# Kernel tuning notes

Hardware: AMD Instinct MI355X
Metric: run time of the kernel (lower is better)

Reference implementation:

```python
import jax, jax.numpy as jnp
import numpy as np

NEG_SLOPE = 0.2


def _add_self_loops(src, dst, edge_attr, n):
    # PyG add_self_loops with fill_value='mean': self-loop attr for node i is the
    # mean of edge_attr over edges whose target is i (0 if none).
    attr_sum = jax.ops.segment_sum(edge_attr, dst, num_segments=n)          # [N,1]
    cnt = jax.ops.segment_sum(jnp.ones((src.shape[0],), edge_attr.dtype), dst, num_segments=n)
    loop_attr = attr_sum / jnp.maximum(cnt, 1.0)[:, None]                   # [N,1]
    loop = jnp.arange(n, dtype=src.dtype)
    return (jnp.concatenate([src, loop]),
            jnp.concatenate([dst, loop]),
            jnp.concatenate([edge_attr, loop_attr], axis=0))


def _gatv2_layer(x, src, dst, eattr, Wl, Wr, We, att, b, n):
    # GATv2Conv (heads=1, concat=False): e_ij = att . leaky_relu(Wl x_j + Wr x_i + We a_ij)
    xl = x @ Wl                                   # [N,C] source transform
    xr = x @ Wr                                   # [N,C] target transform
    ef = eattr @ We                               # [E,C]
    z = jax.nn.leaky_relu(xl[src] + xr[dst] + ef, NEG_SLOPE)   # [E,C]
    logits = z @ att                              # [E]
    # segment softmax over target node dst
    m = jax.ops.segment_max(logits, dst, num_segments=n)
    ex = jnp.exp(logits - m[dst])
    s = jax.ops.segment_sum(ex, dst, num_segments=n)
    alpha = ex / (s[dst] + 1e-16)                 # [E]
    out = jax.ops.segment_sum(alpha[:, None] * xl[src], dst, num_segments=n)  # [N,C]
    return out + b


def setup_inputs() -> dict:
    key = jax.random.key(0)
    ks = jax.random.split(key, 16)
    N, E, F_IN, H, OUT = 50000, 800000, 128, 128, 64
    x = jax.random.normal(ks[0], (N, F_IN), jnp.float32)
    edge_index = jax.random.randint(ks[1], (2, E), 0, N, jnp.int32)
    edge_attr = jax.random.normal(ks[2], (E, 1), jnp.float32)
    s = 0.1
    return {
        "x": x, "edge_index": edge_index, "edge_attr": edge_attr,
        "Wl1": jax.random.normal(ks[3], (F_IN, H), jnp.float32) * s,
        "Wr1": jax.random.normal(ks[4], (F_IN, H), jnp.float32) * s,
        "We1": jax.random.normal(ks[5], (1, H), jnp.float32) * s,
        "att1": jax.random.normal(ks[6], (H,), jnp.float32) * s,
        "b1": jnp.zeros((H,), jnp.float32),
        "Wl2": jax.random.normal(ks[7], (H, OUT), jnp.float32) * s,
        "Wr2": jax.random.normal(ks[8], (H, OUT), jnp.float32) * s,
        "We2": jax.random.normal(ks[9], (1, OUT), jnp.float32) * s,
        "att2": jax.random.normal(ks[10], (OUT,), jnp.float32) * s,
        "b2": jnp.zeros((OUT,), jnp.float32),
    }


def reference(x, edge_index, edge_attr, Wl1, Wr1, We1, att1, b1, Wl2, Wr2, We2, att2, b2):
    n = x.shape[0]
    src, dst, ea = _add_self_loops(edge_index[0], edge_index[1], edge_attr, n)
    h = jax.nn.elu(_gatv2_layer(x, src, dst, ea, Wl1, Wr1, We1, att1, b1, n))
    out = jax.nn.elu(_gatv2_layer(h, src, dst, ea, Wl2, Wr2, We2, att2, b2, n))
    return out
```

## Files before the change

kernel.cpp:

```cpp
#include <hip/hip_runtime.h>
#include <math.h>


#define NEG_SLOPE 0.2f
#define CNT_SHIFT 44
#define SUM_MASK ((1ULL << 44) - 1)
#define ATTR_BIAS 8.0
#define ATTR_SCALE 268435456.0

typedef __attribute__((ext_vector_type(8))) short bf16x8;
typedef __attribute__((ext_vector_type(4))) float f32x4;

__device__ __forceinline__ float bf_lo(unsigned int u) { return __uint_as_float(u << 16); }
__device__ __forceinline__ float bf_hi(unsigned int u) { return __uint_as_float(u & 0xFFFF0000u); }
__device__ __forceinline__ unsigned short bf16_rne(float f) {
    unsigned int u = __float_as_uint(f);
    return (unsigned short)((u + 0x7FFFu + ((u >> 16) & 1u)) >> 16);
}
__device__ __forceinline__ unsigned int pack_bf16(float a, float b) {
    unsigned int ua = __float_as_uint(a);
    unsigned int ub = __float_as_uint(b);
    ua = (ua + 0x7FFFu + ((ua >> 16) & 1u)) >> 16;
    ub = (ub + 0x7FFFu + ((ub >> 16) & 1u)) & 0xFFFF0000u;
    return ua | ub;
}

__global__ void wprep_kernel(const float* __restrict__ Wl1, const float* __restrict__ Wr1,
                             const float* __restrict__ Wl2, const float* __restrict__ Wr2,
                             short* __restrict__ Wt1, short* __restrict__ Wt2) {
    int i = blockIdx.x * 256 + threadIdx.x;
    if (i < 256 * 128) {
        int nn = i >> 7, k = i & 127;
        float v = (nn < 128) ? Wl1[k * 128 + nn] : Wr1[k * 128 + (nn - 128)];
        Wt1[i] = (short)bf16_rne(v);
    } else if (i < 256 * 128 + 128 * 128) {
        int j = i - 256 * 128;
        int nn = j >> 7, k = j & 127;
        float v = (nn < 64) ? Wl2[k * 64 + nn] : Wr2[k * 64 + (nn - 64)];
        Wt2[j] = (short)bf16_rne(v);
    }
}

__global__ void edge_pass1_kernel(const int* __restrict__ dst, const float* __restrict__ eattr,
                                  unsigned long long* __restrict__ packed,
                                  unsigned short* __restrict__ rank, int E) {
    int e = blockIdx.x * blockDim.x + threadIdx.x;
    if (e < E) {
        int d = dst[e];
        double q = ((double)eattr[e] + ATTR_BIAS) * ATTR_SCALE;
        unsigned long long inc = (1ULL << CNT_SHIFT) | (unsigned long long)q;
        unsigned long long old = atomicAdd(&packed[d], inc);
        rank[e] = (unsigned short)(old >> CNT_SHIFT);
    }
}

__global__ __launch_bounds__(1024) void scan_part_kernel(
    const unsigned long long* __restrict__ packed, int* __restrict__ partials, int n) {
    __shared__ int red[1024];
    int gid = blockIdx.x * 1024 + threadIdx.x;
    red[threadIdx.x] = (gid < n) ? ((int)(packed[gid] >> CNT_SHIFT) + 1) : 0;
    __syncthreads();
    for (int off = 512; off > 0; off >>= 1) {
        if (threadIdx.x < off) red[threadIdx.x] += red[threadIdx.x + off];
        __syncthreads();
    }
    if (threadIdx.x == 0) partials[blockIdx.x] = red[0];
}

__global__ __launch_bounds__(1024) void scan_blocksums_kernel(int* __restrict__ partials, int nb) {
    __shared__ int buf[1024];
    int t = threadIdx.x;
    int v = (t < nb) ? partials[t] : 0;
    buf[t] = v;
    __syncthreads();
    for (int off = 1; off < 1024; off <<= 1) {
        int a = (t >= off) ? buf[t - off] : 0;
        __syncthreads();
        buf[t] += a;
        __syncthreads();
    }
    if (t < nb) partials[t] = buf[t] - v;
}

__global__ __launch_bounds__(1024) void scan_final_kernel(
    const unsigned long long* __restrict__ packed, const int* __restrict__ partials,
    int* __restrict__ row_ptr, int n) {
    __shared__ int buf[1024];
    int gid = blockIdx.x * 1024 + threadIdx.x;
    int v = (gid < n) ? ((int)(packed[gid] >> CNT_SHIFT) + 1) : 0;
    buf[threadIdx.x] = v;
    __syncthreads();
    for (int off = 1; off < 1024; off <<= 1) {
        int a = (threadIdx.x >= off) ? buf[threadIdx.x - off] : 0;
        __syncthreads();
        buf[threadIdx.x] += a;
        __syncthreads();
    }
    if (gid < n) row_ptr[gid + 1] = partials[blockIdx.x] + buf[threadIdx.x];
    if (gid == 0) row_ptr[0] = 0;
}

__global__ void csr_scatter_kernel(const int* __restrict__ src, const int* __restrict__ dst,
                                   const float* __restrict__ eattr,
                                   const unsigned long long* __restrict__ packed,
                                   const unsigned short* __restrict__ rank,
                                   const int* __restrict__ row_ptr,
                                   int2* __restrict__ csr, int E, int n) {
    int i = blockIdx.x * blockDim.x + threadIdx.x;
    if (i < E) {
        int d = dst[i];
        csr[row_ptr[d] + rank[i]] = make_int2(src[i], __float_as_int(eattr[i]));
    } else if (i < E + n) {
        int v = i - E;
        unsigned long long p = packed[v];
        int cnt = (int)(p >> CNT_SHIFT);
        double sum = (double)(p & SUM_MASK) * (1.0 / ATTR_SCALE) - ATTR_BIAS * cnt;
        float mean = (cnt > 0) ? (float)(sum / cnt) : 0.f;
        csr[row_ptr[v] + cnt] = make_int2(v, __float_as_int(mean));
    }
}

template <int COUT, int WM, int WN>
__global__ __launch_bounds__(256) void xform_mfma_kernel(
    const float* __restrict__ X, const short* __restrict__ Wt,
    unsigned short* __restrict__ XL, float* __restrict__ XR, int n) {
    constexpr int CIN = 128;
    constexpr int BM = WM * 64;
    constexpr int PITCH = CIN + 8;
    static_assert(WM * WN == 4, "4 waves");
    __shared__ short xs[BM * PITCH];

    const int t = threadIdx.x;
    const int node0 = blockIdx.x * BM;

    constexpr int NF4 = BM * CIN / 4;
    const float4* Xv = (const float4*)(X + (size_t)node0 * CIN);
    for (int idx = t; idx < NF4; idx += 256) {
        int r = idx >> 5;
        int c4 = idx & 31;
        uint2 w;
        if (node0 + r < n) {
            float4 v = Xv[idx];
            w = make_uint2(pack_bf16(v.x, v.y), pack_bf16(v.z, v.w));
        } else {
            w = make_uint2(0u, 0u);
        }
        *(uint2*)(xs + r * PITCH + c4 * 4) = w;
    }
    __syncthreads();

    const int wv = t >> 6, lane = t & 63;
    const int mw = wv / WN, nw = wv % WN;
    const int m0 = mw * 64, n0 = nw * 64;
    const int ln = lane & 15, kg = lane >> 4;

    f32x4 acc[4][4];
#pragma unroll
    for (int i = 0; i < 4; ++i)
#pragma unroll
        for (int j = 0; j < 4; ++j) acc[i][j] = (f32x4){0.f, 0.f, 0.f, 0.f};

#pragma unroll
    for (int ks = 0; ks < 4; ++ks) {
        bf16x8 b[4], a[4];
#pragma unroll
        for (int mt = 0; mt < 4; ++mt)
            b[mt] = *(const bf16x8*)(xs + (m0 + mt * 16 + ln) * PITCH + ks * 32 + kg * 8);
#pragma unroll
        for (int nt = 0; nt < 4; ++nt)
            a[nt] = *(const bf16x8*)(Wt + (size_t)(n0 + nt * 16 + ln) * CIN + ks * 32 + kg * 8);
#pragma unroll
        for (int nt = 0; nt < 4; ++nt)
#pragma unroll
            for (int mt = 0; mt < 4; ++mt)
                acc[nt][mt] = __builtin_amdgcn_mfma_f32_16x16x32_bf16(
                    a[nt], b[mt], acc[nt][mt], 0, 0, 0);
    }

    const bool isXL = (n0 < COUT);
#pragma unroll
    for (int mt = 0; mt < 4; ++mt) {
        int m = node0 + m0 + mt * 16 + ln;
        if (m >= n) continue;
#pragma unroll
        for (int nt = 0; nt < 4; ++nt) {
            f32x4 v = acc[nt][mt];
            int nl = n0 + nt * 16 + kg * 4;
            if (isXL) {
                *(uint2*)(XL + (size_t)m * COUT + nl) =
                    make_uint2(pack_bf16(v.x, v.y), pack_bf16(v.z, v.w));
            } else {
                *(f32x4*)(XR + (size_t)m * COUT + (nl - COUT)) = v;
            }
        }
    }
}

template <int C>
__global__ __launch_bounds__(256) void agg_grouped_kernel(
    const unsigned short* __restrict__ XL, const float* XR,
    const int* __restrict__ row_ptr, const int2* __restrict__ csr,
    const float* __restrict__ We, const float* __restrict__ att,
    const float* __restrict__ bias, float* OUT, int n) {
    constexpr int CPL = C / 16;
    constexpr int NW = CPL / 2;
    constexpr int U = 4;
    const int wave = threadIdx.x >> 6;
    const int lane = threadIdx.x & 63;
    const int node = blockIdx.x * 4 + wave;
    if (node >= n) return;
    const int l16 = lane & 15;
    const int grp = lane >> 4;
    const int cb  = l16 * CPL;

    float wev[CPL], atv[CPL];
#pragma unroll
    for (int j = 0; j < CPL; j += 4) {
        *(float4*)&wev[j] = *(const float4*)(We  + cb + j);
        *(float4*)&atv[j] = *(const float4*)(att + cb + j);
    }

    float xr[CPL];
#pragma unroll
    for (int j = 0; j < CPL; j += 4)
        *(float4*)&xr[j] = *(const float4*)(XR + (size_t)node * C + cb + j);

    const int p0 = row_ptr[node], pe = row_ptr[node + 1];
    float s = 0.f;
    float acc[CPL];
#pragma unroll
    for (int j = 0; j < CPL; ++j) acc[j] = 0.f;

    int p = p0 + grp;
    for (; p + 4 * (U - 1) < pe; p += 4 * U) {
        int2 ed[U];
#pragma unroll
        for (int u = 0; u < U; ++u) ed[u] = csr[p + 4 * u];

        unsigned int uw[U][NW];
#pragma unroll
        for (int u = 0; u < U; ++u) {
            const unsigned short* xlp = XL + (size_t)ed[u].x * C + cb;
            if constexpr (NW == 4) {
                uint4 q = *(const uint4*)xlp;
                uw[u][0] = q.x; uw[u][1] = q.y; uw[u][2] = q.z; uw[u][3] = q.w;
            } else {
                uint2 q = *(const uint2*)xlp;
                uw[u][0] = q.x; uw[u][1] = q.y;
            }
        }

#pragma unroll
        for (int u = 0; u < U; ++u) {
            float xl[CPL];
#pragma unroll
            for (int j2 = 0; j2 < NW; ++j2) {
                xl[2 * j2]     = bf_lo(uw[u][j2]);
                xl[2 * j2 + 1] = bf_hi(uw[u][j2]);
            }
            float ae = __int_as_float(ed[u].y);
            float part = 0.f;
#pragma unroll
            for (int j = 0; j < CPL; ++j) {
                float z = fmaf(ae, wev[j], xr[j]) + xl[j];
                z = fmaxf(z, NEG_SLOPE * z);
                part = fmaf(atv[j], z, part);
            }
#pragma unroll
            for (int off = 1; off < 16; off <<= 1) part += __shfl_xor(part, off, 64);
            float w = __expf(part);
            s += w;
#pragma unroll
            for (int j = 0; j < CPL; ++j) acc[j] = fmaf(w, xl[j], acc[j]);
        }
    }
    for (; p < pe; p += 4) {
        int2 ed = csr[p];
        const unsigned short* xlp = XL + (size_t)ed.x * C + cb;
        unsigned int uw[NW];
        if constexpr (NW == 4) {
            uint4 q = *(const uint4*)xlp;
            uw[0] = q.x; uw[1] = q.y; uw[2] = q.z; uw[3] = q.w;
        } else {
            uint2 q = *(const uint2*)xlp;
            uw[0] = q.x; uw[1] = q.y;
        }
        float xl[CPL];
#pragma unroll
        for (int j2 = 0; j2 < NW; ++j2) {
            xl[2 * j2]     = bf_lo(uw[j2]);
            xl[2 * j2 + 1] = bf_hi(uw[j2]);
        }
        float ae = __int_as_float(ed.y);
        float part = 0.f;
#pragma unroll
        for (int j = 0; j < CPL; ++j) {
            float z = fmaf(ae, wev[j], xr[j]) + xl[j];
            z = fmaxf(z, NEG_SLOPE * z);
            part = fmaf(atv[j], z, part);
        }
#pragma unroll
        for (int off = 1; off < 16; off <<= 1) part += __shfl_xor(part, off, 64);
        float w = __expf(part);
        s += w;
#pragma unroll
        for (int j = 0; j < CPL; ++j) acc[j] = fmaf(w, xl[j], acc[j]);
    }

#pragma unroll
    for (int off = 16; off <= 32; off <<= 1) {
        s += __shfl_xor(s, off, 64);
#pragma unroll
        for (int j = 0; j < CPL; ++j) acc[j] += __shfl_xor(acc[j], off, 64);
    }

    if (grp == 0) {
        float inv = 1.f / (s + 1e-16f);
        float o[CPL];
#pragma unroll
        for (int j = 0; j < CPL; ++j) {
            float v = fmaf(acc[j], inv, bias[cb + j]);
            o[j] = (v > 0.f) ? v : (__expf(v) - 1.f);
        }
#pragma unroll
        for (int j = 0; j < CPL; j += 4)
            *(float4*)(OUT + (size_t)node * C + cb + j) = *(const float4*)&o[j];
    }
}

extern "C" void kernel_launch(void* const* d_in, const int* in_sizes, int n_in,
                              void* d_out, int out_size, void* d_ws, size_t ws_size,
                              hipStream_t stream) {
    const float* x    = (const float*)d_in[0];
    const int*   eidx = (const int*)  d_in[1];
    const float* ea   = (const float*)d_in[2];
    const float* Wl1  = (const float*)d_in[3];
    const float* Wr1  = (const float*)d_in[4];
    const float* We1  = (const float*)d_in[5];
    const float* att1 = (const float*)d_in[6];
    const float* b1   = (const float*)d_in[7];
    const float* Wl2  = (const float*)d_in[8];
    const float* Wr2  = (const float*)d_in[9];
    const float* We2  = (const float*)d_in[10];
    const float* att2 = (const float*)d_in[11];
    const float* b2   = (const float*)d_in[12];

    const int FIN = 128, H = 128, OUTC = 64;
    const int E  = in_sizes[2];
    const int N  = in_sizes[0] / FIN;
    const int EP = E + N;
    const int NB = (N + 1023) / 1024;
    const int* src = eidx;
    const int* dst = eidx + E;

    char* ws = (char*)d_ws;
    size_t off = 0;
    auto alloc = [&](size_t bytes) {
        size_t o = off;
        off += (bytes + 255) & ~(size_t)255;
        return o;
    };
    size_t packed_off = alloc((size_t)N * 8);
    size_t zero_bytes = off;
    size_t rank_off  = alloc((size_t)E * 2);
    size_t rp_off    = alloc((size_t)(N + 1) * 4);
    size_t part_off  = alloc((size_t)NB * 4);
    size_t csr_off   = alloc((size_t)EP * 8);
    size_t wt1_off   = alloc((size_t)256 * 128 * 2);
    size_t wt2_off   = alloc((size_t)128 * 128 * 2);
    size_t xl1_off   = alloc((size_t)N * H * 2);
    size_t xr1_off   = alloc((size_t)N * H * 4);
    size_t xr2_off   = alloc((size_t)N * OUTC * 4);

    unsigned long long* packed = (unsigned long long*)(ws + packed_off);
    unsigned short*     rank   = (unsigned short*)(ws + rank_off);
    int*   rp    = (int*)  (ws + rp_off);
    int*   part  = (int*)  (ws + part_off);
    int2*  csr   = (int2*) (ws + csr_off);
    short* wt1   = (short*)(ws + wt1_off);
    short* wt2   = (short*)(ws + wt2_off);
    unsigned short* xl1 = (unsigned short*)(ws + xl1_off);
    float* xr1   = (float*)(ws + xr1_off);
    float* h     = xr1;
    unsigned short* xl2 = (unsigned short*)(ws + xl1_off);
    float* xr2   = (float*)(ws + xr2_off);

    (void)ws_size; (void)n_in; (void)out_size;

    hipMemsetAsync(ws, 0, zero_bytes, stream);

    const int TB = 256;
    wprep_kernel<<<192, 256, 0, stream>>>(Wl1, Wr1, Wl2, Wr2, wt1, wt2);
    edge_pass1_kernel<<<(E + TB - 1) / TB, TB, 0, stream>>>(dst, ea, packed, rank, E);
    scan_part_kernel<<<NB, 1024, 0, stream>>>(packed, part, N);
    scan_blocksums_kernel<<<1, 1024, 0, stream>>>(part, NB);
    scan_final_kernel<<<NB, 1024, 0, stream>>>(packed, part, rp, N);
    csr_scatter_kernel<<<(EP + TB - 1) / TB, TB, 0, stream>>>(src, dst, ea, packed, rank,
                                                              rp, csr, E, N);
    xform_mfma_kernel<128, 1, 4><<<(N + 63) / 64, 256, 0, stream>>>(x, wt1, xl1, xr1, N);
    agg_grouped_kernel<128><<<(N + 3) / 4, 256, 0, stream>>>(xl1, xr1, rp, csr,
                                                             We1, att1, b1, h, N);
    xform_mfma_kernel<64, 2, 2><<<(N + 127) / 128, 256, 0, stream>>>(h, wt2, xl2, xr2, N);
    agg_grouped_kernel<64><<<(N + 3) / 4, 256, 0, stream>>>(xl2, xr2, rp, csr,
                                                            We2, att2, b2, (float*)d_out, N);
}
```

Baseline: 213.7 us.

## Use persistent grid-stride aggregation with configurable lanes-per-edge and masked unroll

The aggregation kernel becomes persistent: it launches a fixed grid and each wave loops over nodes with a grid stride, so We/att/bias are loaded once per wave rather than once per node. Lanes-per-edge and unroll depth become template parameters. Layer 2 now uses 8 lanes per edge (8 edges in flight per wave, uint4 loads), and layer 1 keeps 16 lanes with an unroll of 4. The scalar tail loop is replaced by a masked unrolled loop that clamps indices and zeroes invalid weights, which adds some wasted gathers on low-degree nodes.

```diff
diff --git a/kernel.cpp b/kernel.cpp
--- a/kernel.cpp
+++ b/kernel.cpp
@@ -196,135 +196,102 @@
     }
 }
 
-template <int C>
+template <int C, int LPE, int U>
 __global__ __launch_bounds__(256) void agg_grouped_kernel(
     const unsigned short* __restrict__ XL, const float* XR,
     const int* __restrict__ row_ptr, const int2* __restrict__ csr,
     const float* __restrict__ We, const float* __restrict__ att,
     const float* __restrict__ bias, float* OUT, int n) {
-    constexpr int CPL = C / 16;
+    constexpr int NGRP = 64 / LPE;
+    constexpr int CPL = C / LPE;
     constexpr int NW = CPL / 2;
-    constexpr int U = 4;
     const int wave = threadIdx.x >> 6;
     const int lane = threadIdx.x & 63;
-    const int node = blockIdx.x * 4 + wave;
-    if (node >= n) return;
-    const int l16 = lane & 15;
-    const int grp = lane >> 4;
-    const int cb  = l16 * CPL;
-
-    float wev[CPL], atv[CPL];
+    const int lg  = lane & (LPE - 1);
+    const int grp = lane / LPE;
+    const int cb  = lg * CPL;
+
+    float wev[CPL], atv[CPL], bv[CPL];
 #pragma unroll
     for (int j = 0; j < CPL; j += 4) {
         *(float4*)&wev[j] = *(const float4*)(We  + cb + j);
         *(float4*)&atv[j] = *(const float4*)(att + cb + j);
-    }
-
-    float xr[CPL];
-#pragma unroll
-    for (int j = 0; j < CPL; j += 4)
-        *(float4*)&xr[j] = *(const float4*)(XR + (size_t)node * C + cb + j);
-
-    const int p0 = row_ptr[node], pe = row_ptr[node + 1];
-    float s = 0.f;
-    float acc[CPL];
-#pragma unroll
-    for (int j = 0; j < CPL; ++j) acc[j] = 0.f;
-
-    int p = p0 + grp;
-    for (; p + 4 * (U - 1) < pe; p += 4 * U) {
-        int2 ed[U];
-#pragma unroll
-        for (int u = 0; u < U; ++u) ed[u] = csr[p + 4 * u];
-
-        unsigned int uw[U][NW];
-#pragma unroll
-        for (int u = 0; u < U; ++u) {
-            const unsigned short* xlp = XL + (size_t)ed[u].x * C + cb;
-            if constexpr (NW == 4) {
-                uint4 q = *(const uint4*)xlp;
+        *(float4*)&bv[j]  = *(const float4*)(bias + cb + j);
+    }
+
+    const int stride = gridDim.x * 4;
+    for (int node = blockIdx.x * 4 + wave; node < n; node += stride) {
+        float xr[CPL];
+#pragma unroll
+        for (int j = 0; j < CPL; j += 4)
+            *(float4*)&xr[j] = *(const float4*)(XR + (size_t)node * C + cb + j);
+
+        const int p0 = row_ptr[node], pe = row_ptr[node + 1];
+        float s = 0.f;
+        float acc[CPL];
+#pragma unroll
+        for (int j = 0; j < CPL; ++j) acc[j] = 0.f;
+
+        for (int base = p0 + grp; base < pe; base += NGRP * U) {
+            int2 ed[U];
+            bool valid[U];
+#pragma unroll
+            for (int u = 0; u < U; ++u) {
+                int p = base + u * NGRP;
+                valid[u] = (p < pe);
+                ed[u] = csr[valid[u] ? p : (pe - 1)];
+            }
+            unsigned int uw[U][NW];
+#pragma unroll
+            for (int u = 0; u < U; ++u) {
+                uint4 q = *(const uint4*)(XL + (size_t)ed[u].x * C + cb);
                 uw[u][0] = q.x; uw[u][1] = q.y; uw[u][2] = q.z; uw[u][3] = q.w;
-            } else {
-                uint2 q = *(const uint2*)xlp;
-                uw[u][0] = q.x; uw[u][1] = q.y;
-            }
-        }
-
-#pragma unroll
-        for (int u = 0; u < U; ++u) {
-            float xl[CPL];
-#pragma unroll
-            for (int j2 = 0; j2 < NW; ++j2) {
-                xl[2 * j2]     = bf_lo(uw[u][j2]);
-                xl[2 * j2 + 1] = bf_hi(uw[u][j2]);
-            }
-            float ae = __int_as_float(ed[u].y);
-            float part = 0.f;
+            }
+#pragma unroll
+            for (int u = 0; u < U; ++u) {
+                float xl[CPL];
+#pragma unroll
+                for (int j2 = 0; j2 < NW; ++j2) {
+                    xl[2 * j2]     = bf_lo(uw[u][j2]);
+                    xl[2 * j2 + 1] = bf_hi(uw[u][j2]);
+                }
+                float ae = __int_as_float(ed[u].y);
+                float part = 0.f;
+#pragma unroll
+                for (int j = 0; j < CPL; ++j) {
+                    float z = fmaf(ae, wev[j], xr[j]) + xl[j];
+                    z = fmaxf(z, NEG_SLOPE * z);
+                    part = fmaf(atv[j], z, part);
+                }
+#pragma unroll
+                for (int off = 1; off < LPE; off <<= 1)
+                    part += __shfl_xor(part, off, 64);
+                float w = valid[u] ? __expf(part) : 0.f;
+                s += w;
+#pragma unroll
+                for (int j = 0; j < CPL; ++j) acc[j] = fmaf(w, xl[j], acc[j]);
+            }
+        }
+
+#pragma unroll
+        for (int off = LPE; off < 64; off <<= 1) {
+            s += __shfl_xor(s, off, 64);
+#pragma unroll
+            for (int j = 0; j < CPL; ++j) acc[j] += __shfl_xor(acc[j], off, 64);
+        }
+
+        if (grp == 0) {
+            float inv = 1.f / (s + 1e-16f);
+            float o[CPL];
 #pragma unroll
             for (int j = 0; j < CPL; ++j) {
-                float z = fmaf(ae, wev[j], xr[j]) + xl[j];
-                z = fmaxf(z, NEG_SLOPE * z);
-                part = fmaf(atv[j], z, part);
-            }
-#pragma unroll
-            for (int off = 1; off < 16; off <<= 1) part += __shfl_xor(part, off, 64);
-            float w = __expf(part);
-            s += w;
-#pragma unroll
-            for (int j = 0; j < CPL; ++j) acc[j] = fmaf(w, xl[j], acc[j]);
-        }
-    }
-    for (; p < pe; p += 4) {
-        int2 ed = csr[p];
-        const unsigned short* xlp = XL + (size_t)ed.x * C + cb;
-        unsigned int uw[NW];
-        if constexpr (NW == 4) {
-            uint4 q = *(const uint4*)xlp;
-            uw[0] = q.x; uw[1] = q.y; uw[2] = q.z; uw[3] = q.w;
-        } else {
-            uint2 q = *(const uint2*)xlp;
-            uw[0] = q.x; uw[1] = q.y;
-        }
-        float xl[CPL];
-#pragma unroll
-        for (int j2 = 0; j2 < NW; ++j2) {
-            xl[2 * j2]     = bf_lo(uw[j2]);
-            xl[2 * j2 + 1] = bf_hi(uw[j2]);
-        }
-        float ae = __int_as_float(ed.y);
-        float part = 0.f;
-#pragma unroll
-        for (int j = 0; j < CPL; ++j) {
-            float z = fmaf(ae, wev[j], xr[j]) + xl[j];
-            z = fmaxf(z, NEG_SLOPE * z);
-            part = fmaf(atv[j], z, part);
-        }
-#pragma unroll
-        for (int off = 1; off < 16; off <<= 1) part += __shfl_xor(part, off, 64);
-        float w = __expf(part);
-        s += w;
-#pragma unroll
-        for (int j = 0; j < CPL; ++j) acc[j] = fmaf(w, xl[j], acc[j]);
-    }
-
-#pragma unroll
-    for (int off = 16; off <= 32; off <<= 1) {
-        s += __shfl_xor(s, off, 64);
-#pragma unroll
-        for (int j = 0; j < CPL; ++j) acc[j] += __shfl_xor(acc[j], off, 64);
-    }
-
-    if (grp == 0) {
-        float inv = 1.f / (s + 1e-16f);
-        float o[CPL];
-#pragma unroll
-        for (int j = 0; j < CPL; ++j) {
-            float v = fmaf(acc[j], inv, bias[cb + j]);
-            o[j] = (v > 0.f) ? v : (__expf(v) - 1.f);
-        }
-#pragma unroll
-        for (int j = 0; j < CPL; j += 4)
-            *(float4*)(OUT + (size_t)node * C + cb + j) = *(const float4*)&o[j];
+                float v = fmaf(acc[j], inv, bv[j]);
+                o[j] = (v > 0.f) ? v : (__expf(v) - 1.f);
+            }
+#pragma unroll
+            for (int j = 0; j < CPL; j += 4)
+                *(float4*)(OUT + (size_t)node * C + cb + j) = *(const float4*)&o[j];
+        }
     }
 }
 
@@ -390,6 +357,7 @@
     hipMemsetAsync(ws, 0, zero_bytes, stream);
 
     const int TB = 256;
+    const int AGG_BLOCKS = 2048;
     wprep_kernel<<<192, 256, 0, stream>>>(Wl1, Wr1, Wl2, Wr2, wt1, wt2);
     edge_pass1_kernel<<<(E + TB - 1) / TB, TB, 0, stream>>>(dst, ea, packed, rank, E);
     scan_part_kernel<<<NB, 1024, 0, stream>>>(packed, part, N);
@@ -398,9 +366,9 @@
     csr_scatter_kernel<<<(EP + TB - 1) / TB, TB, 0, stream>>>(src, dst, ea, packed, rank,
                                                               rp, csr, E, N);
     xform_mfma_kernel<128, 1, 4><<<(N + 63) / 64, 256, 0, stream>>>(x, wt1, xl1, xr1, N);
-    agg_grouped_kernel<128><<<(N + 3) / 4, 256, 0, stream>>>(xl1, xr1, rp, csr,
-                                                             We1, att1, b1, h, N);
+    agg_grouped_kernel<128, 16, 4><<<AGG_BLOCKS, 256, 0, stream>>>(xl1, xr1, rp, csr,
+                                                                   We1, att1, b1, h, N);
     xform_mfma_kernel<64, 2, 2><<<(N + 127) / 128, 256, 0, stream>>>(h, wt2, xl2, xr2, N);
-    agg_grouped_kernel<64><<<(N + 3) / 4, 256, 0, stream>>>(xl2, xr2, rp, csr,
-                                                            We2, att2, b2, (float*)d_out, N);
-}
+    agg_grouped_kernel<64, 8, 2><<<AGG_BLOCKS, 256, 0, stream>>>(xl2, xr2, rp, csr,
+                                                                 We2, att2, b2, (float*)d_out, N);
+}
```

Result: no change. 216.1 us (+1.1%).
